# Performance work log

Hardware: AMD Instinct MI355X
Metric: run time of the kernel (lower is better)

## Reference

```python
import jax, jax.numpy as jnp
import numpy as np

MAX_SEQ = 768  # hardcoded in original compute_freqs_cis
THETA = 10000.0


def _freqs_cis(C, T):
    # freqs over FULL embed dim C (matches original, not per-head)
    freqs = 1.0 / THETA ** (jnp.arange(0, C, 2, dtype=jnp.float32)[: C // 2] / C)
    t = jnp.arange(MAX_SEQ, dtype=jnp.float32)
    ang = jnp.outer(t, freqs)  # [MAX_SEQ, C/2]
    return jnp.cos(ang)[:T], jnp.sin(ang)[:T]  # each [T, C/2]


def _apply_rope(u):
    # u: [B, T, C]; rotate adjacent channel pairs across full C
    B, T, C = u.shape
    fr, fi = _freqs_cis(C, T)           # [T, C/2]
    u2 = u.astype(jnp.float32).reshape(B, T, C // 2, 2)
    ur, ui = u2[..., 0], u2[..., 1]     # [B, T, C/2]
    out_r = ur * fr - ui * fi
    out_i = ur * fi + ui * fr
    return jnp.stack([out_r, out_i], axis=-1).reshape(B, T, C).astype(u.dtype)


def setup_inputs() -> dict:
    key = jax.random.key(0)
    k1, k2, k3 = jax.random.split(key, 3)
    B, T, C = 16, 768, 1024
    x = jax.random.normal(k1, (B, T, C), dtype=jnp.float32)
    Wqkv = jax.random.normal(k2, (3 * C, C), dtype=jnp.float32) * 0.02
    bqkv = jnp.zeros((3 * C,), dtype=jnp.float32)
    Wo = jax.random.normal(k3, (C, C), dtype=jnp.float32) * 0.02
    bo = jnp.zeros((C,), dtype=jnp.float32)
    return {"x": x, "Wqkv": Wqkv, "bqkv": bqkv, "Wo": Wo, "bo": bo}


def reference(x, Wqkv, bqkv, Wo, bo):
    B, T, C = x.shape
    H = 16
    D = C // H
    qkv = x @ Wqkv.T + bqkv                      # [B, T, 3C]
    q, k, v = jnp.split(qkv, 3, axis=-1)
    q = _apply_rope(q)
    k = _apply_rope(k)
    # [B, H, T, D]
    q = q.reshape(B, T, H, D).transpose(0, 2, 1, 3)
    k = k.reshape(B, T, H, D).transpose(0, 2, 1, 3)
    v = v.reshape(B, T, H, D).transpose(0, 2, 1, 3)
    scale = 1.0 / jnp.sqrt(jnp.asarray(D, dtype=q.dtype))
    scores = jnp.einsum("bhqd,bhkd->bhqk", q, k) * scale
    causal = jnp.tril(jnp.ones((T, T), dtype=bool))
    scores = jnp.where(causal, scores, jnp.finfo(scores.dtype).min)
    attn = jax.nn.softmax(scores, axis=-1)
    y = jnp.einsum("bhqk,bhkd->bhqd", attn, v)   # [B, H, T, D]
    y = y.transpose(0, 2, 1, 3).reshape(B, T, C)
    return y @ Wo.T + bo
```

## Files before the change

kernel.cpp:

```cpp
#include <hip/hip_runtime.h>
#include <hip/hip_bf16.h>

typedef __attribute__((ext_vector_type(8))) short bf16x8;
typedef __attribute__((ext_vector_type(4))) float f32x4;
typedef unsigned short u16;
typedef unsigned int u32;

#define DEV __device__ __forceinline__

DEV float bf2f(u16 v) { u32 u = ((u32)v) << 16; return __builtin_bit_cast(float, u); }
DEV u16 f2bf(float f) {
    u32 u = __builtin_bit_cast(u32, f);
    u32 r = (u + 0x7FFFu + ((u >> 16) & 1u)) >> 16;
    return (u16)r;
}

DEV void gll16(const u16* g, u16* l) {
    __builtin_amdgcn_global_load_lds((const __attribute__((address_space(1))) void*)g,
                                     (__attribute__((address_space(3))) void*)l, 16, 0, 0);
}

#define WAIT_VM0()   asm volatile("s_waitcnt vmcnt(0)" ::: "memory")
#define WAIT_LGKM0() asm volatile("s_waitcnt lgkmcnt(0)" ::: "memory")
#define BAR()        __builtin_amdgcn_s_barrier()
#define BARF()       asm volatile("s_barrier" ::: "memory")

__global__ void detect_kernel(const u32* __restrict__ x, int* __restrict__ flag) {
    __shared__ int cnt;
    if (threadIdx.x == 0) cnt = 0;
    __syncthreads();
    int c = 0;
    for (int i = threadIdx.x; i < 4096; i += 256) {
        u32 w = x[i];
        u32 e = (w >> 7) & 0xFF;
        c += (e >= 110 && e <= 132) ? 1 : 0;
    }
    atomicAdd(&cnt, c);
    __syncthreads();
    if (threadIdx.x == 0) *flag = (cnt * 2 > 4096) ? 1 : 0;
}

__global__ void cvt_bf16_kernel(const void* __restrict__ in, u16* __restrict__ out,
                                int n8, const int* __restrict__ flag) {
    const int fl = *flag;
    int i = blockIdx.x * 256 + threadIdx.x;
    const int stride = gridDim.x * 256;
    if (fl) {
        const bf16x8* ip = (const bf16x8*)in;
        bf16x8* op = (bf16x8*)out;
        for (; i < n8; i += stride) op[i] = ip[i];
    } else {
        const float4* ip = (const float4*)in;
        bf16x8* op = (bf16x8*)out;
        for (; i < n8; i += stride) {
            float4 a = ip[2 * i], b = ip[2 * i + 1];
            bf16x8 o;
            o[0] = (short)f2bf(a.x); o[1] = (short)f2bf(a.y);
            o[2] = (short)f2bf(a.z); o[3] = (short)f2bf(a.w);
            o[4] = (short)f2bf(b.x); o[5] = (short)f2bf(b.y);
            o[6] = (short)f2bf(b.z); o[7] = (short)f2bf(b.w);
            op[i] = o;
        }
    }
}

__global__ void cvt_f32_kernel(const void* __restrict__ in, float* __restrict__ out,
                               int n, const int* __restrict__ flag) {
    const int fl = *flag;
    int i = blockIdx.x * 256 + threadIdx.x;
    if (i < n) out[i] = fl ? bf2f(((const u16*)in)[i]) : ((const float*)in)[i];
}

__global__ void rope_table_kernel(float2* __restrict__ tab) {
    int idx = blockIdx.x * 256 + threadIdx.x;
    int t = idx >> 9, j = idx & 511;
    float freq = expf(-(float)(2 * j) * (9.210340371976184f / 1024.0f));
    float ang = (float)t * freq;
    tab[idx] = make_float2(cosf(ang), sinf(ang));
}

__global__ __launch_bounds__(512, 2)
void gemm256p_kernel(const u16* __restrict__ A, const u16* __restrict__ W,
                     const float* __restrict__ bias, void* __restrict__ C,
                     int N, const int* __restrict__ flag, int out_mode,
                     const float2* __restrict__ tab, int rope) {
    constexpr int K = 1024, NT = 16;
    __shared__ u16 lds[2][32768];
    const int tid = threadIdx.x;
    const int l = tid & 63, w = tid >> 6;
    const int wm = w >> 2, wn = w & 3;
    const int lo = l & 15, hi = l >> 4;

    const int M0 = blockIdx.x * 256, N0 = blockIdx.y * 256;

    const int rS = tid >> 3;
    const int qS = (tid & 7) ^ (rS & 7);
    const u16* Ag = A + (size_t)(M0 + rS) * K + qS * 8;
    const u16* Wg = W + (size_t)(N0 + rS) * K + qS * 8;
    const int lb = w * 512;

    f32x4 acc[8][4] = {};

#define STG_A(kt, slot, half)                                                  \
    {                                                                          \
        u16* sA_ = &lds[slot][(half) * 8192];                                  \
        const u16* ga_ = Ag + (kt) * 64 + (size_t)(128 * (half)) * K;          \
        gll16(ga_,                  sA_ + lb);                                 \
        gll16(ga_ + (size_t)64 * K, sA_ + 4096 + lb);                          \
    }
#define STG_B(kt, slot, half)                                                  \
    {                                                                          \
        u16* sB_ = &lds[slot][16384 + (half) * 8192];                          \
        const u16* gb_ = Wg + (kt) * 64 + (size_t)(128 * (half)) * K;          \
        gll16(gb_,                  sB_ + lb);                                 \
        gll16(gb_ + (size_t)64 * K, sB_ + 4096 + lb);                          \
    }

    STG_A(0, 0, 0); STG_A(0, 0, 1);
    STG_B(0, 0, 0); STG_B(0, 0, 1);
    WAIT_VM0();
    BARF();

    const int csw = lo & 7;

#pragma unroll 1
    for (int t = 0; t < NT; ++t) {
        const int cur = t & 1, nxt = cur ^ 1;
        const u16* sA = &lds[cur][0];
        const u16* sB = &lds[cur][16384];
        bf16x8 afr[4], bfr[4];

#pragma unroll
        for (int n = 0; n < 4; ++n)
            bfr[n] = *(const bf16x8*)&sB[(wn * 64 + n * 16 + lo) * 64 + ((hi ^ csw) * 8)];
#pragma unroll
        for (int m = 0; m < 4; ++m)
            afr[m] = *(const bf16x8*)&sA[(wm * 128 + m * 16 + lo) * 64 + ((hi ^ csw) * 8)];
        if (t + 1 < NT) { STG_A(t + 1, nxt, 0); STG_A(t + 1, nxt, 1); }
        BARF();
        __builtin_amdgcn_s_setprio(1);
#pragma unroll
        for (int m = 0; m < 4; ++m)
#pragma unroll
            for (int n = 0; n < 4; ++n)
                acc[m][n] = __builtin_amdgcn_mfma_f32_16x16x32_bf16(afr[m], bfr[n], acc[m][n], 0, 0, 0);
        __builtin_amdgcn_s_setprio(0);
        BARF();

#pragma unroll
        for (int m = 0; m < 4; ++m)
            afr[m] = *(const bf16x8*)&sA[(wm * 128 + 64 + m * 16 + lo) * 64 + ((hi ^ csw) * 8)];
        if (t + 1 < NT) { STG_B(t + 1, nxt, 0); STG_B(t + 1, nxt, 1); }
        BARF();
        __builtin_amdgcn_s_setprio(1);
#pragma unroll
        for (int m = 0; m < 4; ++m)
#pragma unroll
            for (int n = 0; n < 4; ++n)
                acc[4 + m][n] = __builtin_amdgcn_mfma_f32_16x16x32_bf16(afr[m], bfr[n], acc[4 + m][n], 0, 0, 0);
        __builtin_amdgcn_s_setprio(0);
        BARF();

#pragma unroll
        for (int n = 0; n < 4; ++n)
            bfr[n] = *(const bf16x8*)&sB[(wn * 64 + n * 16 + lo) * 64 + (((4 + hi) ^ csw) * 8)];
#pragma unroll
        for (int m = 0; m < 4; ++m)
            afr[m] = *(const bf16x8*)&sA[(wm * 128 + m * 16 + lo) * 64 + (((4 + hi) ^ csw) * 8)];
        BARF();
        __builtin_amdgcn_s_setprio(1);
#pragma unroll
        for (int m = 0; m < 4; ++m)
#pragma unroll
            for (int n = 0; n < 4; ++n)
                acc[m][n] = __builtin_amdgcn_mfma_f32_16x16x32_bf16(afr[m], bfr[n], acc[m][n], 0, 0, 0);
        __builtin_amdgcn_s_setprio(0);
        BARF();

#pragma unroll
        for (int m = 0; m < 4; ++m)
            afr[m] = *(const bf16x8*)&sA[(wm * 128 + 64 + m * 16 + lo) * 64 + (((4 + hi) ^ csw) * 8)];
        WAIT_VM0();
        BARF();
        __builtin_amdgcn_s_setprio(1);
#pragma unroll
        for (int m = 0; m < 4; ++m)
#pragma unroll
            for (int n = 0; n < 4; ++n)
                acc[4 + m][n] = __builtin_amdgcn_mfma_f32_16x16x32_bf16(afr[m], bfr[n], acc[4 + m][n], 0, 0, 0);
        __builtin_amdgcn_s_setprio(0);
        BARF();
    }
#undef STG_A
#undef STG_B

    const int f32out = out_mode ? (*flag == 0) : 0;
    const int do_rope = rope && (N0 < 2048);
#pragma unroll
    for (int mi = 0; mi < 8; ++mi) {
        const int rbase = M0 + wm * 128 + (mi >> 2) * 64 + (mi & 3) * 16 + hi * 4;
        const int tbase = (M0 % 768) + wm * 128 + (mi >> 2) * 64 + (mi & 3) * 16 + hi * 4;
#pragma unroll
        for (int n = 0; n < 4; ++n) {
            const int col = N0 + wn * 64 + lo + n * 16;
            float bi = bias[col];
            const int jf = (col & 1023) >> 1;
            const int odd = col & 1;
#pragma unroll
            for (int j = 0; j < 4; ++j) {
                float v = acc[mi][n][j] + bi;
                if (do_rope) {
                    float partner = __shfl_xor(v, 1);
                    float2 cs = tab[(tbase + j) * 512 + jf];
                    v = odd ? (v * cs.x + partner * cs.y) : (v * cs.x - partner * cs.y);
                }
                size_t idx = (size_t)(rbase + j) * N + col;
                if (f32out) ((float*)C)[idx] = v;
                else        ((u16*)C)[idx] = f2bf(v);
            }
        }
    }
}

__global__ __launch_bounds__(512)
void attn_kernel(const u16* __restrict__ qkv, u16* __restrict__ y) {
    constexpr int T = 768, CH = 1024, QKVC = 3072;
    constexpr float NEG = -30000.0f;
    __shared__ u16 Ks[2][64 * 64];
    __shared__ u16 Vt[64 * 72];
    __shared__ u16 Ps[128 * 72];

    const int tid = threadIdx.x, l = tid & 63, w = tid >> 6;
    const int qt = blockIdx.x, h = blockIdx.y, b = blockIdx.z;
    const int lo = l & 15, hi = l >> 4;
    const int kk = hi * 8;
    const int swzk = (lo & 7) * 8;

    const int qrow = qt * 128 + w * 16 + lo;
    const u16* qptr = qkv + (size_t)(b * T + qrow) * QKVC + h * 64 + kk;
    bf16x8 aq0r = *(const bf16x8*)qptr;
    bf16x8 aq1r = *(const bf16x8*)(qptr + 32);
    bf16x8 aq0, aq1;
#pragma unroll
    for (int e = 0; e < 8; ++e) {
        aq0[e] = (short)f2bf(bf2f((u16)aq0r[e]) * 0.125f);
        aq1[e] = (short)f2bf(bf2f((u16)aq1r[e]) * 0.125f);
    }

    f32x4 o[4] = {};
    float mrun[4] = {NEG, NEG, NEG, NEG};
    float lrun[4] = {0.f, 0.f, 0.f, 0.f};

    const int ksr = w * 8 + (l >> 3);
    const int ksc = ((l & 7) ^ ((l >> 3) & 7)) * 8;
    const u16* kbase = qkv + (size_t)(b * T + ksr) * QKVC + CH + h * 64 + ksc;

    const int vd0 = (tid & 7) * 8;
    const int vswz = (tid & 7) * 8;
    const int vr0 = tid >> 3;
    const u16* vbase = qkv + (size_t)(b * T) * QKVC + 2 * CH + h * 64 + vd0;

    const int NTk = 2 * qt + 2;

    gll16(kbase, &Ks[0][w * 512]);
    bf16x8 cv0 = *(const bf16x8*)(vbase + (size_t)vr0 * QKVC);
    WAIT_VM0();
#pragma unroll
    for (int e = 0; e < 8; ++e)
        Vt[(vd0 + e) * 72 + (vr0 ^ vswz)] = (u16)cv0[e];

    for (int kt = 0; kt < NTk; ++kt) {
        const int cur = kt & 1, nxt = cur ^ 1;
        bf16x8 nv0;
        if (kt + 1 < NTk) {
            const size_t koff = (size_t)((kt + 1) * 64) * QKVC;
            gll16(kbase + koff, &Ks[nxt][w * 512]);
            nv0 = *(const bf16x8*)(vbase + (size_t)((kt + 1) * 64 + vr0) * QKVC);
        }
        WAIT_LGKM0();
        BAR();

        __builtin_amdgcn_s_setprio(1);
        f32x4 s[4];
#pragma unroll
        for (int n = 0; n < 4; ++n) {
            bf16x8 kb0 = *(const bf16x8*)&Ks[cur][(n * 16 + lo) * 64 + (kk ^ swzk)];
            bf16x8 kb1 = *(const bf16x8*)&Ks[cur][(n * 16 + lo) * 64 + ((32 + kk) ^ swzk)];
            f32x4 z = {0.f, 0.f, 0.f, 0.f};
            z = __builtin_amdgcn_mfma_f32_16x16x32_bf16(aq0, kb0, z, 0, 0, 0);
            z = __builtin_amdgcn_mfma_f32_16x16x32_bf16(aq1, kb1, z, 0, 0, 0);
            s[n] = z;
        }
        __builtin_amdgcn_s_setprio(0);

        if (kt >= 2 * qt) {
#pragma unroll
            for (int n = 0; n < 4; ++n) {
                int kcol = kt * 64 + n * 16 + lo;
#pragma unroll
                for (int j = 0; j < 4; ++j)
                    if (kcol > qt * 128 + w * 16 + hi * 4 + j) s[n][j] = NEG;
            }
        }
        float mnew[4], corr[4];
#pragma unroll
        for (int j = 0; j < 4; ++j) {
            float mx = fmaxf(fmaxf(s[0][j], s[1][j]), fmaxf(s[2][j], s[3][j]));
            mx = fmaxf(mx, __shfl_xor(mx, 1));
            mx = fmaxf(mx, __shfl_xor(mx, 2));
            mx = fmaxf(mx, __shfl_xor(mx, 4));
            mx = fmaxf(mx, __shfl_xor(mx, 8));
            mnew[j] = fmaxf(mrun[j], mx);
            corr[j] = __expf(mrun[j] - mnew[j]);
            mrun[j] = mnew[j];
        }
        float p[4][4];
#pragma unroll
        for (int n = 0; n < 4; ++n)
#pragma unroll
            for (int j = 0; j < 4; ++j)
                p[n][j] = __expf(s[n][j] - mnew[j]);
#pragma unroll
        for (int j = 0; j < 4; ++j) {
            float r = p[0][j] + p[1][j] + p[2][j] + p[3][j];
            r += __shfl_xor(r, 1);
            r += __shfl_xor(r, 2);
            r += __shfl_xor(r, 4);
            r += __shfl_xor(r, 8);
            lrun[j] = lrun[j] * corr[j] + r;
        }
#pragma unroll
        for (int n = 0; n < 4; ++n)
#pragma unroll
            for (int j = 0; j < 4; ++j)
                o[n][j] *= corr[j];
#pragma unroll
        for (int n = 0; n < 4; ++n)
#pragma unroll
            for (int j = 0; j < 4; ++j)
                Ps[(w * 16 + hi * 4 + j) * 72 + n * 16 + lo] = f2bf(p[n][j]);

        __builtin_amdgcn_s_setprio(1);
#pragma unroll
        for (int c = 0; c < 2; ++c) {
            bf16x8 pa = *(const bf16x8*)&Ps[(w * 16 + lo) * 72 + c * 32 + kk];
#pragma unroll
            for (int n = 0; n < 4; ++n) {
                const int v = (n * 2 + (lo >> 3)) & 7;
                bf16x8 vb = *(const bf16x8*)&Vt[(n * 16 + lo) * 72 + ((c * 32 + kk) ^ (v * 8))];
                o[n] = __builtin_amdgcn_mfma_f32_16x16x32_bf16(pa, vb, o[n], 0, 0, 0);
            }
        }
        __builtin_amdgcn_s_setprio(0);

        if (kt + 1 < NTk) {
            WAIT_VM0();
            BAR();
#pragma unroll
            for (int e = 0; e < 8; ++e)
                Vt[(vd0 + e) * 72 + (vr0 ^ vswz)] = (u16)nv0[e];
        }
    }

    float inv[4];
#pragma unroll
    for (int j = 0; j < 4; ++j) inv[j] = (lrun[j] > 0.f) ? 1.0f / lrun[j] : 0.f;
#pragma unroll
    for (int n = 0; n < 4; ++n)
#pragma unroll
        for (int j = 0; j < 4; ++j) {
            int t = qt * 128 + w * 16 + hi * 4 + j;
            y[(size_t)(b * T + t) * CH + h * 64 + n * 16 + lo] = f2bf(o[n][j] * inv[j]);
        }
}

extern "C" void kernel_launch(void* const* d_in, const int* in_sizes, int n_in,
                              void* d_out, int out_size, void* d_ws, size_t ws_size,
                              hipStream_t stream) {
    char* ws = (char*)d_ws;
    int*   flag  = (int*)ws;
    u16*   xb    = (u16*)(ws + 256);
    u16*   Wqb   = (u16*)(ws + 256 + 25165824);
    u16*   Wob   = (u16*)(ws + 256 + 31457280);
    float* bqf   = (float*)(ws + 256 + 33554432);
    float* bof   = (float*)(ws + 256 + 33566720);
    u16*   qkv   = (u16*)(ws + 256 + 33570816);
    u16*   y     = (u16*)(ws + 256 + 109068288);
    float2* tab  = (float2*)(ws + 256 + 134234112);

    detect_kernel<<<1, 256, 0, stream>>>((const u32*)d_in[0], flag);
    cvt_bf16_kernel<<<2048, 256, 0, stream>>>(d_in[0], xb,  12582912 / 8, flag);
    cvt_bf16_kernel<<<1536, 256, 0, stream>>>(d_in[1], Wqb, 3145728 / 8, flag);
    cvt_bf16_kernel<<<512,  256, 0, stream>>>(d_in[3], Wob, 1048576 / 8, flag);
    cvt_f32_kernel<<<12, 256, 0, stream>>>(d_in[2], bqf, 3072, flag);
    cvt_f32_kernel<<<4,  256, 0, stream>>>(d_in[4], bof, 1024, flag);
    rope_table_kernel<<<768 * 512 / 256, 256, 0, stream>>>(tab);

    gemm256p_kernel<<<dim3(48, 12), 512, 0, stream>>>(xb, Wqb, bqf, qkv, 3072, flag, 0, tab, 1);
    attn_kernel<<<dim3(6, 16, 16), 512, 0, stream>>>(qkv, y);
    gemm256p_kernel<<<dim3(48, 4), 512, 0, stream>>>(y, Wob, bof, d_out, 1024, flag, 1, tab, 0);
}
```

Baseline: 302.9 us.

## Switch GEMM to triple-buffered BK=32 pipeline with two-stage prefetch

Replaces the double-buffered BK=64 main loop of the GEMM with a three-slot ring of BK=32 tiles. Each slot is staged two iterations ahead, and partial vmcnt waits let one stage's loads stay in flight. LDS use drops from 128KB to 96KB per block, and the swizzle is adapted to 32-element rows. The aim is to hide global-to-LDS latency better. The cost is twice as many loop iterations and barriers per K step, with fewer MFMAs between barriers.

```diff
diff --git a/kernel.cpp b/kernel.cpp
--- a/kernel.cpp
+++ b/kernel.cpp
@@ -21,6 +21,7 @@
 }
 
 #define WAIT_VM0()   asm volatile("s_waitcnt vmcnt(0)" ::: "memory")
+#define WAIT_VM4()   asm volatile("s_waitcnt vmcnt(4)" ::: "memory")
 #define WAIT_LGKM0() asm volatile("s_waitcnt lgkmcnt(0)" ::: "memory")
 #define BAR()        __builtin_amdgcn_s_barrier()
 #define BARF()       asm volatile("s_barrier" ::: "memory")
@@ -80,12 +81,12 @@
 }
 
 __global__ __launch_bounds__(512, 2)
-void gemm256p_kernel(const u16* __restrict__ A, const u16* __restrict__ W,
+void gemm256c_kernel(const u16* __restrict__ A, const u16* __restrict__ W,
                      const float* __restrict__ bias, void* __restrict__ C,
                      int N, const int* __restrict__ flag, int out_mode,
                      const float2* __restrict__ tab, int rope) {
-    constexpr int K = 1024, NT = 16;
-    __shared__ u16 lds[2][32768];
+    constexpr int K = 1024, NT = 32;
+    __shared__ u16 lds[3][16384];
     const int tid = threadIdx.x;
     const int l = tid & 63, w = tid >> 6;
     const int wm = w >> 2, wn = w & 3;
@@ -93,50 +94,46 @@
 
     const int M0 = blockIdx.x * 256, N0 = blockIdx.y * 256;
 
-    const int rS = tid >> 3;
-    const int qS = (tid & 7) ^ (rS & 7);
+    const int rS = tid >> 2;
+    const int qS = (tid & 3) ^ ((tid >> 3) & 3);
     const u16* Ag = A + (size_t)(M0 + rS) * K + qS * 8;
     const u16* Wg = W + (size_t)(N0 + rS) * K + qS * 8;
     const int lb = w * 512;
 
     f32x4 acc[8][4] = {};
 
-#define STG_A(kt, slot, half)                                                  \
+#define STAGE(kt, slot)                                                        \
     {                                                                          \
-        u16* sA_ = &lds[slot][(half) * 8192];                                  \
-        const u16* ga_ = Ag + (kt) * 64 + (size_t)(128 * (half)) * K;          \
-        gll16(ga_,                  sA_ + lb);                                 \
-        gll16(ga_ + (size_t)64 * K, sA_ + 4096 + lb);                          \
-    }
-#define STG_B(kt, slot, half)                                                  \
-    {                                                                          \
-        u16* sB_ = &lds[slot][16384 + (half) * 8192];                          \
-        const u16* gb_ = Wg + (kt) * 64 + (size_t)(128 * (half)) * K;          \
-        gll16(gb_,                  sB_ + lb);                                 \
-        gll16(gb_ + (size_t)64 * K, sB_ + 4096 + lb);                          \
-    }
-
-    STG_A(0, 0, 0); STG_A(0, 0, 1);
-    STG_B(0, 0, 0); STG_B(0, 0, 1);
-    WAIT_VM0();
+        u16* sA_ = &lds[slot][0];                                              \
+        u16* sB_ = &lds[slot][8192];                                           \
+        const u16* ga_ = Ag + (kt) * 32;                                       \
+        const u16* gb_ = Wg + (kt) * 32;                                       \
+        gll16(ga_,                   sA_ + lb);                                \
+        gll16(ga_ + (size_t)128 * K, sA_ + 4096 + lb);                         \
+        gll16(gb_,                   sB_ + lb);                                \
+        gll16(gb_ + (size_t)128 * K, sB_ + 4096 + lb);                         \
+    }
+
+    STAGE(0, 0);
+    STAGE(1, 1);
+    WAIT_VM4();
     BARF();
 
-    const int csw = lo & 7;
+    const int csw = (lo & 7) >> 1;
 
 #pragma unroll 1
     for (int t = 0; t < NT; ++t) {
-        const int cur = t & 1, nxt = cur ^ 1;
-        const u16* sA = &lds[cur][0];
-        const u16* sB = &lds[cur][16384];
+        const u16* sA = &lds[t % 3][0];
+        const u16* sB = &lds[t % 3][8192];
         bf16x8 afr[4], bfr[4];
 
 #pragma unroll
         for (int n = 0; n < 4; ++n)
-            bfr[n] = *(const bf16x8*)&sB[(wn * 64 + n * 16 + lo) * 64 + ((hi ^ csw) * 8)];
+            bfr[n] = *(const bf16x8*)&sB[(wn * 64 + n * 16 + lo) * 32 + ((hi ^ csw) * 8)];
 #pragma unroll
         for (int m = 0; m < 4; ++m)
-            afr[m] = *(const bf16x8*)&sA[(wm * 128 + m * 16 + lo) * 64 + ((hi ^ csw) * 8)];
-        if (t + 1 < NT) { STG_A(t + 1, nxt, 0); STG_A(t + 1, nxt, 1); }
+            afr[m] = *(const bf16x8*)&sA[(wm * 128 + m * 16 + lo) * 32 + ((hi ^ csw) * 8)];
+        if (t + 2 < NT) STAGE(t + 2, (t + 2) % 3);
         BARF();
         __builtin_amdgcn_s_setprio(1);
 #pragma unroll
@@ -149,8 +146,11 @@
 
 #pragma unroll
         for (int m = 0; m < 4; ++m)
-            afr[m] = *(const bf16x8*)&sA[(wm * 128 + 64 + m * 16 + lo) * 64 + ((hi ^ csw) * 8)];
-        if (t + 1 < NT) { STG_B(t + 1, nxt, 0); STG_B(t + 1, nxt, 1); }
+            afr[m] = *(const bf16x8*)&sA[(wm * 128 + 64 + m * 16 + lo) * 32 + ((hi ^ csw) * 8)];
+        if (t + 1 < NT) {
+            if (t + 2 < NT) { WAIT_VM4(); }
+            else            { WAIT_VM0(); }
+        }
         BARF();
         __builtin_amdgcn_s_setprio(1);
 #pragma unroll
@@ -160,39 +160,8 @@
                 acc[4 + m][n] = __builtin_amdgcn_mfma_f32_16x16x32_bf16(afr[m], bfr[n], acc[4 + m][n], 0, 0, 0);
         __builtin_amdgcn_s_setprio(0);
         BARF();
-
-#pragma unroll
-        for (int n = 0; n < 4; ++n)
-            bfr[n] = *(const bf16x8*)&sB[(wn * 64 + n * 16 + lo) * 64 + (((4 + hi) ^ csw) * 8)];
-#pragma unroll
-        for (int m = 0; m < 4; ++m)
-            afr[m] = *(const bf16x8*)&sA[(wm * 128 + m * 16 + lo) * 64 + (((4 + hi) ^ csw) * 8)];
-        BARF();
-        __builtin_amdgcn_s_setprio(1);
-#pragma unroll
-        for (int m = 0; m < 4; ++m)
-#pragma unroll
-            for (int n = 0; n < 4; ++n)
-                acc[m][n] = __builtin_amdgcn_mfma_f32_16x16x32_bf16(afr[m], bfr[n], acc[m][n], 0, 0, 0);
-        __builtin_amdgcn_s_setprio(0);
-        BARF();
-
-#pragma unroll
-        for (int m = 0; m < 4; ++m)
-            afr[m] = *(const bf16x8*)&sA[(wm * 128 + 64 + m * 16 + lo) * 64 + (((4 + hi) ^ csw) * 8)];
-        WAIT_VM0();
-        BARF();
-        __builtin_amdgcn_s_setprio(1);
-#pragma unroll
-        for (int m = 0; m < 4; ++m)
-#pragma unroll
-            for (int n = 0; n < 4; ++n)
-                acc[4 + m][n] = __builtin_amdgcn_mfma_f32_16x16x32_bf16(afr[m], bfr[n], acc[4 + m][n], 0, 0, 0);
-        __builtin_amdgcn_s_setprio(0);
-        BARF();
-    }
-#undef STG_A
-#undef STG_B
+    }
+#undef STAGE
 
     const int f32out = out_mode ? (*flag == 0) : 0;
     const int do_rope = rope && (N0 < 2048);
@@ -396,7 +365,7 @@
     cvt_f32_kernel<<<4,  256, 0, stream>>>(d_in[4], bof, 1024, flag);
     rope_table_kernel<<<768 * 512 / 256, 256, 0, stream>>>(tab);
 
-    gemm256p_kernel<<<dim3(48, 12), 512, 0, stream>>>(xb, Wqb, bqf, qkv, 3072, flag, 0, tab, 1);
+    gemm256c_kernel<<<dim3(48, 12), 512, 0, stream>>>(xb, Wqb, bqf, qkv, 3072, flag, 0, tab, 1);
     attn_kernel<<<dim3(6, 16, 16), 512, 0, stream>>>(qkv, y);
-    gemm256p_kernel<<<dim3(48, 4), 512, 0, stream>>>(y, Wob, bof, d_out, 1024, flag, 1, tab, 0);
-}
+    gemm256c_kernel<<<dim3(48, 4), 512, 0, stream>>>(y, Wob, bof, d_out, 1024, flag, 1, tab, 0);
+}
```

Result: no change. 307.8 us (+1.6%).

## Use lazy softmax rescaling, deferred row-sum reduction, and fuse bias conversion into GEMM

Applied to the files above, without the earlier changes.

Rewrites the online softmax in the attention kernel so the running max and rescale of output and row sum happen only when some row's max grows by more than a threshold (checked wave-wide). The per-tile cross-lane row-sum shuffles move to a single reduction at the end. P is stored to LDS with truncation instead of round-to-nearest. Separately, the two bias conversion launches are removed and the GEMM epilogue reads bias directly based on the dtype flag. The risks are lower precision from truncation and a larger exponent range in p when the max is not updated.

```diff
diff --git a/kernel.cpp b/kernel.cpp
--- a/kernel.cpp
+++ b/kernel.cpp
@@ -14,6 +14,7 @@
     u32 r = (u + 0x7FFFu + ((u >> 16) & 1u)) >> 16;
     return (u16)r;
 }
+DEV u16 f2bf_trunc(float f) { return (u16)(__builtin_bit_cast(u32, f) >> 16); }
 
 DEV void gll16(const u16* g, u16* l) {
     __builtin_amdgcn_global_load_lds((const __attribute__((address_space(1))) void*)g,
@@ -64,13 +65,6 @@
     }
 }
 
-__global__ void cvt_f32_kernel(const void* __restrict__ in, float* __restrict__ out,
-                               int n, const int* __restrict__ flag) {
-    const int fl = *flag;
-    int i = blockIdx.x * 256 + threadIdx.x;
-    if (i < n) out[i] = fl ? bf2f(((const u16*)in)[i]) : ((const float*)in)[i];
-}
-
 __global__ void rope_table_kernel(float2* __restrict__ tab) {
     int idx = blockIdx.x * 256 + threadIdx.x;
     int t = idx >> 9, j = idx & 511;
@@ -81,7 +75,7 @@
 
 __global__ __launch_bounds__(512, 2)
 void gemm256p_kernel(const u16* __restrict__ A, const u16* __restrict__ W,
-                     const float* __restrict__ bias, void* __restrict__ C,
+                     const void* __restrict__ bias, void* __restrict__ C,
                      int N, const int* __restrict__ flag, int out_mode,
                      const float2* __restrict__ tab, int rope) {
     constexpr int K = 1024, NT = 16;
@@ -194,7 +188,8 @@
 #undef STG_A
 #undef STG_B
 
-    const int f32out = out_mode ? (*flag == 0) : 0;
+    const int fl = *flag;
+    const int f32out = out_mode ? (fl == 0) : 0;
     const int do_rope = rope && (N0 < 2048);
 #pragma unroll
     for (int mi = 0; mi < 8; ++mi) {
@@ -203,7 +198,7 @@
 #pragma unroll
         for (int n = 0; n < 4; ++n) {
             const int col = N0 + wn * 64 + lo + n * 16;
-            float bi = bias[col];
+            float bi = fl ? bf2f(((const u16*)bias)[col]) : ((const float*)bias)[col];
             const int jf = (col & 1023) >> 1;
             const int odd = col & 1;
 #pragma unroll
@@ -302,43 +297,40 @@
                     if (kcol > qt * 128 + w * 16 + hi * 4 + j) s[n][j] = NEG;
             }
         }
-        float mnew[4], corr[4];
+        float mx[4];
 #pragma unroll
         for (int j = 0; j < 4; ++j) {
-            float mx = fmaxf(fmaxf(s[0][j], s[1][j]), fmaxf(s[2][j], s[3][j]));
-            mx = fmaxf(mx, __shfl_xor(mx, 1));
-            mx = fmaxf(mx, __shfl_xor(mx, 2));
-            mx = fmaxf(mx, __shfl_xor(mx, 4));
-            mx = fmaxf(mx, __shfl_xor(mx, 8));
-            mnew[j] = fmaxf(mrun[j], mx);
-            corr[j] = __expf(mrun[j] - mnew[j]);
-            mrun[j] = mnew[j];
+            float m0 = fmaxf(fmaxf(s[0][j], s[1][j]), fmaxf(s[2][j], s[3][j]));
+            m0 = fmaxf(m0, __shfl_xor(m0, 1));
+            m0 = fmaxf(m0, __shfl_xor(m0, 2));
+            m0 = fmaxf(m0, __shfl_xor(m0, 4));
+            m0 = fmaxf(m0, __shfl_xor(m0, 8));
+            mx[j] = m0;
+        }
+        float g = fmaxf(fmaxf(mx[0] - mrun[0], mx[1] - mrun[1]),
+                        fmaxf(mx[2] - mrun[2], mx[3] - mrun[3]));
+        if (!__all(g <= 8.0f)) {
+#pragma unroll
+            for (int j = 0; j < 4; ++j) {
+                float mn = fmaxf(mrun[j], mx[j]);
+                float c = __expf(mrun[j] - mn);
+                mrun[j] = mn;
+                lrun[j] *= c;
+#pragma unroll
+                for (int n = 0; n < 4; ++n) o[n][j] *= c;
+            }
         }
         float p[4][4];
 #pragma unroll
         for (int n = 0; n < 4; ++n)
 #pragma unroll
-            for (int j = 0; j < 4; ++j)
-                p[n][j] = __expf(s[n][j] - mnew[j]);
-#pragma unroll
-        for (int j = 0; j < 4; ++j) {
-            float r = p[0][j] + p[1][j] + p[2][j] + p[3][j];
-            r += __shfl_xor(r, 1);
-            r += __shfl_xor(r, 2);
-            r += __shfl_xor(r, 4);
-            r += __shfl_xor(r, 8);
-            lrun[j] = lrun[j] * corr[j] + r;
-        }
-#pragma unroll
-        for (int n = 0; n < 4; ++n)
-#pragma unroll
-            for (int j = 0; j < 4; ++j)
-                o[n][j] *= corr[j];
-#pragma unroll
-        for (int n = 0; n < 4; ++n)
-#pragma unroll
-            for (int j = 0; j < 4; ++j)
-                Ps[(w * 16 + hi * 4 + j) * 72 + n * 16 + lo] = f2bf(p[n][j]);
+            for (int j = 0; j < 4; ++j) {
+                p[n][j] = __expf(s[n][j] - mrun[j]);
+                Ps[(w * 16 + hi * 4 + j) * 72 + n * 16 + lo] = f2bf_trunc(p[n][j]);
+            }
+#pragma unroll
+        for (int j = 0; j < 4; ++j)
+            lrun[j] += p[0][j] + p[1][j] + p[2][j] + p[3][j];
 
         __builtin_amdgcn_s_setprio(1);
 #pragma unroll
@@ -364,7 +356,14 @@
 
     float inv[4];
 #pragma unroll
-    for (int j = 0; j < 4; ++j) inv[j] = (lrun[j] > 0.f) ? 1.0f / lrun[j] : 0.f;
+    for (int j = 0; j < 4; ++j) {
+        float r = lrun[j];
+        r += __shfl_xor(r, 1);
+        r += __shfl_xor(r, 2);
+        r += __shfl_xor(r, 4);
+        r += __shfl_xor(r, 8);
+        inv[j] = (r > 0.f) ? 1.0f / r : 0.f;
+    }
 #pragma unroll
     for (int n = 0; n < 4; ++n)
 #pragma unroll
@@ -382,8 +381,6 @@
     u16*   xb    = (u16*)(ws + 256);
     u16*   Wqb   = (u16*)(ws + 256 + 25165824);
     u16*   Wob   = (u16*)(ws + 256 + 31457280);
-    float* bqf   = (float*)(ws + 256 + 33554432);
-    float* bof   = (float*)(ws + 256 + 33566720);
     u16*   qkv   = (u16*)(ws + 256 + 33570816);
     u16*   y     = (u16*)(ws + 256 + 109068288);
     float2* tab  = (float2*)(ws + 256 + 134234112);
@@ -392,11 +389,9 @@
     cvt_bf16_kernel<<<2048, 256, 0, stream>>>(d_in[0], xb,  12582912 / 8, flag);
     cvt_bf16_kernel<<<1536, 256, 0, stream>>>(d_in[1], Wqb, 3145728 / 8, flag);
     cvt_bf16_kernel<<<512,  256, 0, stream>>>(d_in[3], Wob, 1048576 / 8, flag);
-    cvt_f32_kernel<<<12, 256, 0, stream>>>(d_in[2], bqf, 3072, flag);
-    cvt_f32_kernel<<<4,  256, 0, stream>>>(d_in[4], bof, 1024, flag);
     rope_table_kernel<<<768 * 512 / 256, 256, 0, stream>>>(tab);
 
-    gemm256p_kernel<<<dim3(48, 12), 512, 0, stream>>>(xb, Wqb, bqf, qkv, 3072, flag, 0, tab, 1);
+    gemm256p_kernel<<<dim3(48, 12), 512, 0, stream>>>(xb, Wqb, d_in[2], qkv, 3072, flag, 0, tab, 1);
     attn_kernel<<<dim3(6, 16, 16), 512, 0, stream>>>(qkv, y);
-    gemm256p_kernel<<<dim3(48, 4), 512, 0, stream>>>(y, Wob, bof, d_out, 1024, flag, 1, tab, 0);
-}
+    gemm256p_kernel<<<dim3(48, 4), 512, 0, stream>>>(y, Wob, d_in[4], d_out, 1024, flag, 1, tab, 0);
+}
```

Measured after the change: 291.0 us. 1.04x faster.
